# Kernel tuning notes

Measured on AMD Instinct MI355X. Metric: run time of the kernel, lower is better.

The kernel has to match this reference:

```python
import jax, jax.numpy as jnp
import numpy as np

B, S, H, L, V = 32, 128, 1024, 2, 32000


def setup_inputs() -> dict:
    key = jax.random.key(0)
    ks = jax.random.split(key, 9)
    scale = 1.0 / np.sqrt(H)
    return {
        "x": jax.random.randint(ks[0], (B, 1), 0, V),
        "hidden": jax.random.normal(ks[1], (L, B, H), jnp.float32) * 0.1,
        "cell": jax.random.normal(ks[2], (L, B, H), jnp.float32) * 0.1,
        "target": jax.random.randint(ks[3], (B, S), 0, V),
        "tf_ratio": 1,  # teacher forcing always on -> deterministic
        "emb": jax.random.normal(ks[4], (V, H), jnp.float32) * 0.02,
        "w_ih": jax.random.normal(ks[5], (L, 4 * H, H), jnp.float32) * scale,
        "w_hh": jax.random.normal(ks[6], (L, 4 * H, H), jnp.float32) * scale,
        "b_ih": jax.random.normal(ks[7], (L, 4 * H), jnp.float32) * scale,
        "b_hh": jax.random.normal(ks[8], (L, 4 * H), jnp.float32) * scale,
    }


def _lstm_decode(tokens, h0, c0, emb, w_ih, w_hh, b_ih, b_hh):
    # tokens: [B,S] int; embed all teacher-forced inputs at once
    x_seq = emb[tokens]                      # [B,S,H]
    x_tbh = jnp.swapaxes(x_seq, 0, 1)        # [S,B,H]
    n_layers = h0.shape[0]

    def step(carry, x_t):
        h, c = carry                         # each [L,B,H]
        inp = x_t                            # [B,H]
        hs, cs = [], []
        for l in range(n_layers):
            # PyTorch gate order: i, f, g, o
            z = inp @ w_ih[l].T + h[l] @ w_hh[l].T + b_ih[l] + b_hh[l]
            i, f, g, o = jnp.split(z, 4, axis=-1)
            c_new = jax.nn.sigmoid(f) * c[l] + jax.nn.sigmoid(i) * jnp.tanh(g)
            h_new = jax.nn.sigmoid(o) * jnp.tanh(c_new)
            hs.append(h_new)
            cs.append(c_new)
            inp = h_new
        return (jnp.stack(hs), jnp.stack(cs)), inp

    _, outs = jax.lax.scan(step, (h0, c0), x_tbh)  # outs: [S,B,H]
    out = jnp.swapaxes(outs, 0, 1)                 # [B,S,H]
    # tied-weight projection to vocab
    return jnp.einsum("bsh,vh->bsv", out, emb)     # [B,S,V]


def reference(x, hidden, cell, target, tf_ratio, emb, w_ih, w_hh, b_ih, b_hh):
    # tf_ratio == 1: step 0 consumes x, step i>=1 consumes target[:, i]
    tokens = jnp.concatenate([x, target[:, 1:]], axis=1)  # [B,S]
    return _lstm_decode(tokens, hidden, cell, emb, w_ih, w_hh, b_ih, b_hh)
```

## Files before the change

### kernel.cpp

```cpp
#include <hip/hip_runtime.h>
#include <stdint.h>


typedef __attribute__((ext_vector_type(8))) short short8;
typedef __attribute__((ext_vector_type(4))) float f32x4;

#define MFMA16(a, b, c) __builtin_amdgcn_mfma_f32_16x16x32_bf16((a), (b), (c), 0, 0, 0)

__device__ __forceinline__ unsigned short f2bf(float f) {
  union { float f; unsigned int u; } v; v.f = f;
  unsigned int u = v.u;
  return (unsigned short)((u + 0x7fffu + ((u >> 16) & 1u)) >> 16);
}

__device__ __forceinline__ void gload_lds16(const unsigned short* g, unsigned short* l) {
  __builtin_amdgcn_global_load_lds(
      (const __attribute__((address_space(1))) void*)g,
      (__attribute__((address_space(3))) void*)l, 16, 0, 0);
}

__device__ __forceinline__ void st_u32_dev(unsigned* p, unsigned v) {
  __hip_atomic_store(p, v, __ATOMIC_RELAXED, __HIP_MEMORY_SCOPE_AGENT);
}
__device__ __forceinline__ unsigned ld_u32_dev(const unsigned* p) {
  return __hip_atomic_load(p, __ATOMIC_RELAXED, __HIP_MEMORY_SCOPE_AGENT);
}


__global__ void cvt_bf16_k(const float* __restrict__ s, unsigned short* __restrict__ d, int n4) {
  int i = blockIdx.x * blockDim.x + threadIdx.x;
  int st = gridDim.x * blockDim.x;
  for (; i < n4; i += st) {
    float4 v = ((const float4*)s)[i];
    ushort4 o;
    o.x = f2bf(v.x); o.y = f2bf(v.y); o.z = f2bf(v.z); o.w = f2bf(v.w);
    ((ushort4*)d)[i] = o;
  }
}

__global__ void bias_sum_k(const float* __restrict__ a, const float* __restrict__ b,
                           float* __restrict__ o, int n) {
  int i = blockIdx.x * blockDim.x + threadIdx.x;
  if (i < n) o[i] = a[i] + b[i];
}

__global__ void embed_k(const int* __restrict__ x, const int* __restrict__ tgt,
                        const float* __restrict__ emb, unsigned short* __restrict__ xseq) {
  int row = blockIdx.x;
  int t = row >> 5, b = row & 31;
  int tok = (t == 0) ? x[b] : tgt[b * 128 + t];
  const float4* e = (const float4*)(emb + (size_t)tok * 1024);
  ushort4* o = (ushort4*)(xseq + (size_t)row * 1024);
  int i = threadIdx.x;
  float4 v = e[i];
  ushort4 u;
  u.x = f2bf(v.x); u.y = f2bf(v.y); u.z = f2bf(v.z); u.w = f2bf(v.w);
  o[i] = u;
}


__global__ __launch_bounds__(256, 2) void gemm_bf16_k(
    const unsigned short* __restrict__ A, const unsigned short* __restrict__ B,
    float* __restrict__ C, const float* __restrict__ bias, int N) {
  __shared__ __align__(16) unsigned short smem[32768];
  const int tid = threadIdx.x;
  const int lane = tid & 63;
  const int w = tid >> 6;
  const int wm = w >> 1, wn = w & 1;
  const int xcd = blockIdx.x & 7;
  const int idx = blockIdx.x >> 3;
  const int nBase = (idx >> 2) * 128;
  const int mBase = (xcd * 4 + (idx & 3)) * 128;
  const int lr = lane & 15, lk = lane >> 4;
  const int K = 1024;

  const int srow = tid >> 3;
  const int scol = (tid & 7) ^ (srow & 7);
  const int wchunk = tid & 192;

  f32x4 acc[4][4];
#pragma unroll
  for (int i = 0; i < 4; ++i)
#pragma unroll
    for (int j = 0; j < 4; ++j) acc[i][j] = (f32x4){0.f, 0.f, 0.f, 0.f};

  const unsigned short* Ag = A + (size_t)mBase * K;
  const unsigned short* Bg = B + (size_t)nBase * K;

  auto stage = [&](int buf, int kt) {
    unsigned short* Ab = smem + buf * 16384;
    unsigned short* Bb = Ab + 8192;
#pragma unroll
    for (int r = 0; r < 4; ++r) {
      int row = r * 32 + srow;
      const unsigned short* ga = Ag + (size_t)row * K + kt * 64 + scol * 8;
      const unsigned short* gb = Bg + (size_t)row * K + kt * 64 + scol * 8;
      gload_lds16(ga, &Ab[(r * 256 + wchunk) * 8]);
      gload_lds16(gb, &Bb[(r * 256 + wchunk) * 8]);
    }
  };

  stage(0, 0);
  __syncthreads();
  for (int kt = 0; kt < 16; ++kt) {
    int cur = kt & 1;
    if (kt < 15) stage(cur ^ 1, kt + 1);
    const unsigned short* Ac = smem + cur * 16384;
    const unsigned short* Bc = Ac + 8192;
#pragma unroll
    for (int ks = 0; ks < 2; ++ks) {
      short8 a[4], b[4];
#pragma unroll
      for (int mf = 0; mf < 4; ++mf) {
        int row = wm * 64 + mf * 16 + lr;
        int cc = (ks * 4 + lk) ^ (row & 7);
        a[mf] = *(const short8*)&Ac[row * 64 + cc * 8];
      }
#pragma unroll
      for (int nf = 0; nf < 4; ++nf) {
        int row = wn * 64 + nf * 16 + lr;
        int cc = (ks * 4 + lk) ^ (row & 7);
        b[nf] = *(const short8*)&Bc[row * 64 + cc * 8];
      }
#pragma unroll
      for (int mf = 0; mf < 4; ++mf)
#pragma unroll
        for (int nf = 0; nf < 4; ++nf)
          acc[mf][nf] = MFMA16(a[mf], b[nf], acc[mf][nf]);
    }
    __syncthreads();
  }

  float* cst = (float*)smem;
#pragma unroll
  for (int r = 0; r < 4; ++r) {
    __syncthreads();
#pragma unroll
    for (int nf = 0; nf < 4; ++nf) {
      int col = wn * 64 + nf * 16 + lr;
      float bv = bias ? bias[nBase + col] : 0.f;
#pragma unroll
      for (int i = 0; i < 4; ++i)
        cst[(wm * 16 + lk * 4 + i) * 132 + col] = acc[r][nf][i] + bv;
    }
    __syncthreads();
#pragma unroll
    for (int pss = 0; pss < 4; ++pss) {
      int idxq = pss * 256 + tid;
      int rl = idxq >> 5, cq = idxq & 31;
      int grow = mBase + (rl >> 4) * 64 + r * 16 + (rl & 15);
      f32x4 v = *(const f32x4*)&cst[rl * 132 + cq * 4];
      __builtin_nontemporal_store(v, (f32x4*)&C[(size_t)grow * N + nBase + cq * 4]);
    }
  }
}


struct PParams {
  const float* zx0;
  const unsigned short* whh0;
  const unsigned short* wih1;
  const unsigned short* whh1;
  const float* bsum1;
  const float* cell;
  unsigned short* h0hist;
  const unsigned short* h1init;
  unsigned short* outb;
  unsigned int* slots0;
  unsigned int* slots1;
};

__global__ __launch_bounds__(512, 1) void lstm_persist_k(PParams P) {
  const int tid = threadIdx.x;
  const int lane = tid & 63;
  const int w = tid >> 6;
  const int lr = lane & 15, lkk = lane >> 4;

  __shared__ __align__(16) unsigned short wlds[65536];
  __shared__ float zraw[4608];

  if (blockIdx.x < 64) {
    const int u0 = blockIdx.x * 16;
    const int m = w >> 2;
    const int gp = (w >> 1) & 1;
    const int kh = w & 1;
    const int g0 = gp * 2, g1 = gp * 2 + 1;

    for (int f = w; f < 128; f += 8) {
      int gg = f >> 5, kc = f & 31;
      const unsigned short* src =
          P.whh0 + (size_t)(gg * 1024 + u0 + lr) * 1024 + kc * 32 + lkk * 8;
      *(short8*)&wlds[f * 512 + lane * 8] = *(const short8*)src;
    }
    const int fb = tid >> 3;
    const int jp = tid & 7;
    float creg[2] = {0.f, 0.f};
    if (tid < 256) {
      creg[0] = P.cell[fb * 1024 + u0 + 2 * jp];
      creg[1] = P.cell[fb * 1024 + u0 + 2 * jp + 1];
    }
    __syncthreads();

    for (int i = 0; i < 128; ++i) {
      if (i > 0 && tid < 64) {
        const unsigned tgt = (unsigned)i;
        while (true) {
          unsigned v = ld_u32_dev(&P.slots0[tid * 32]);
          if (__all(v >= tgt)) break;
          __builtin_amdgcn_s_sleep(1);
        }
      }
      __syncthreads();

      float2 zr[4];
      if (tid < 256) {
        const float2* br = (const float2*)(P.zx0 + (size_t)i * 131072 + fb * 4096 + u0 + 2 * jp);
#pragma unroll
        for (int q = 0; q < 4; ++q) zr[q] = br[q * 512];
      }
      f32x4 acc0 = {0.f, 0.f, 0.f, 0.f}, acc1 = {0.f, 0.f, 0.f, 0.f};
      const unsigned short* ap =
          P.h0hist + (size_t)i * 32768 + (size_t)(m * 16 + lr) * 1024 + kh * 512 + lkk * 8;
#pragma unroll
      for (int g4 = 0; g4 < 2; ++g4) {
        short8 a[8];
#pragma unroll
        for (int q = 0; q < 8; ++q) a[q] = *(const short8*)(ap + (g4 * 8 + q) * 32);
#pragma unroll
        for (int q = 0; q < 8; ++q) {
          int kc = kh * 16 + g4 * 8 + q;
          short8 b0 = *(const short8*)&wlds[(g0 * 32 + kc) * 512 + lane * 8];
          short8 b1 = *(const short8*)&wlds[(g1 * 32 + kc) * 512 + lane * 8];
          acc0 = MFMA16(a[q], b0, acc0);
          acc1 = MFMA16(a[q], b1, acc1);
        }
      }
#pragma unroll
      for (int j = 0; j < 4; ++j) {
        zraw[(kh * 32 + m * 16 + lkk * 4 + j) * 72 + g0 * 16 + lr] = acc0[j];
        zraw[(kh * 32 + m * 16 + lkk * 4 + j) * 72 + g1 * 16 + lr] = acc1[j];
      }
      __syncthreads();

      if (tid < 256) {
        unsigned hv = 0;
#pragma unroll
        for (int u = 0; u < 2; ++u) {
          int j = 2 * jp + u;
          float zi = zraw[fb * 72 + j]      + zraw[(32 + fb) * 72 + j]      + ((u == 0) ? zr[0].x : zr[0].y);
          float zf = zraw[fb * 72 + 16 + j] + zraw[(32 + fb) * 72 + 16 + j] + ((u == 0) ? zr[1].x : zr[1].y);
          float zg = zraw[fb * 72 + 32 + j] + zraw[(32 + fb) * 72 + 32 + j] + ((u == 0) ? zr[2].x : zr[2].y);
          float zo = zraw[fb * 72 + 48 + j] + zraw[(32 + fb) * 72 + 48 + j] + ((u == 0) ? zr[3].x : zr[3].y);
          float ii = 1.f / (1.f + __expf(-zi));
          float ff = 1.f / (1.f + __expf(-zf));
          float gg = tanhf(zg);
          float oo = 1.f / (1.f + __expf(-zo));
          float cn = ff * creg[u] + ii * gg;
          creg[u] = cn;
          float hn = oo * tanhf(cn);
          hv |= ((unsigned)f2bf(hn)) << (16 * u);
        }
        st_u32_dev((unsigned*)&P.h0hist[(size_t)(i + 1) * 32768 + fb * 1024 + u0 + 2 * jp], hv);
      }
      __syncthreads();
      if (tid == 0) st_u32_dev(&P.slots0[blockIdx.x * 32], (unsigned)(i + 1));
    }
  } else {
    const int u0 = (blockIdx.x - 64) * 8;
    const int slot = blockIdx.x - 64;
    const int mat = w >> 2;
    const int m = (w >> 1) & 1;
    const int kh = w & 1;

    for (int f = w; f < 128; f += 8) {
      int matf = f >> 6, nt = (f >> 5) & 1, kc = f & 31;
      int rr = nt * 16 + lr;
      int gate = rr >> 3, unit = rr & 7;
      const unsigned short* Wm = matf ? P.whh1 : P.wih1;
      const unsigned short* src =
          Wm + (size_t)(gate * 1024 + u0 + unit) * 1024 + kc * 32 + lkk * 8;
      *(short8*)&wlds[f * 512 + lane * 8] = *(const short8*)src;
    }
    const int fb = tid >> 2;
    const int jp = tid & 3;
    float creg[2] = {0.f, 0.f};
    float brg[4][2];
    if (tid < 128) {
      creg[0] = P.cell[32768 + fb * 1024 + u0 + 2 * jp];
      creg[1] = P.cell[32768 + fb * 1024 + u0 + 2 * jp + 1];
#pragma unroll
      for (int q = 0; q < 4; ++q) {
        brg[q][0] = P.bsum1[q * 1024 + u0 + 2 * jp];
        brg[q][1] = P.bsum1[q * 1024 + u0 + 2 * jp + 1];
      }
    }
    __syncthreads();

    for (int i = 1; i <= 128; ++i) {
      if (tid < 64) {
        const unsigned t0 = (unsigned)i, t1 = (unsigned)(i - 1);
        while (true) {
          bool ok = ld_u32_dev(&P.slots0[tid * 32]) >= t0;
          if (i > 1) {
            ok = ok && ld_u32_dev(&P.slots1[tid * 32]) >= t1
                    && ld_u32_dev(&P.slots1[(tid + 64) * 32]) >= t1;
          }
          if (__all(ok)) break;
          __builtin_amdgcn_s_sleep(2);
        }
      }
      __syncthreads();

      f32x4 acc0 = {0.f, 0.f, 0.f, 0.f}, acc1 = {0.f, 0.f, 0.f, 0.f};
      const unsigned short* ap;
      if (mat == 0) {
        ap = P.h0hist + (size_t)i * 32768 + (size_t)(m * 16 + lr) * 1024 + kh * 512 + lkk * 8;
      } else {
        size_t h1s = (i == 1) ? 1024 : 131072;
        const unsigned short* h1b =
            (i == 1) ? P.h1init : (P.outb + (size_t)(i - 2) * 1024);
        ap = h1b + (size_t)(m * 16 + lr) * h1s + kh * 512 + lkk * 8;
      }
#pragma unroll
      for (int g4 = 0; g4 < 2; ++g4) {
        short8 a[8];
#pragma unroll
        for (int q = 0; q < 8; ++q) a[q] = *(const short8*)(ap + (g4 * 8 + q) * 32);
#pragma unroll
        for (int q = 0; q < 8; ++q) {
          int kc = kh * 16 + g4 * 8 + q;
          short8 b0 = *(const short8*)&wlds[(mat * 64 + 0 * 32 + kc) * 512 + lane * 8];
          short8 b1 = *(const short8*)&wlds[(mat * 64 + 1 * 32 + kc) * 512 + lane * 8];
          acc0 = MFMA16(a[q], b0, acc0);
          acc1 = MFMA16(a[q], b1, acc1);
        }
      }
      float* zp = zraw + (mat * 2 + kh) * 1152;
#pragma unroll
      for (int j = 0; j < 4; ++j) {
        zp[(m * 16 + lkk * 4 + j) * 36 + lr] = acc0[j];
        zp[(m * 16 + lkk * 4 + j) * 36 + 16 + lr] = acc1[j];
      }
      __syncthreads();

      if (tid < 128) {
        unsigned hv = 0;
#pragma unroll
        for (int u = 0; u < 2; ++u) {
          int j = 2 * jp + u;
          float z4[4];
#pragma unroll
          for (int q = 0; q < 4; ++q) {
            z4[q] = zraw[fb * 36 + q * 8 + j] + zraw[1152 + fb * 36 + q * 8 + j]
                  + zraw[2304 + fb * 36 + q * 8 + j] + zraw[3456 + fb * 36 + q * 8 + j]
                  + brg[q][u];
          }
          float ii = 1.f / (1.f + __expf(-z4[0]));
          float ff = 1.f / (1.f + __expf(-z4[1]));
          float gg = tanhf(z4[2]);
          float oo = 1.f / (1.f + __expf(-z4[3]));
          float cn = ff * creg[u] + ii * gg;
          creg[u] = cn;
          float hn = oo * tanhf(cn);
          hv |= ((unsigned)f2bf(hn)) << (16 * u);
        }
        st_u32_dev((unsigned*)&P.outb[(size_t)fb * 131072 + (size_t)(i - 1) * 1024 + u0 + 2 * jp], hv);
      }
      __syncthreads();
      if (tid == 0) st_u32_dev(&P.slots1[slot * 32], (unsigned)i);
    }
  }
}


extern "C" void kernel_launch(void* const* d_in, const int* in_sizes, int n_in,
                              void* d_out, int out_size, void* d_ws, size_t ws_size,
                              hipStream_t stream) {
  const int*   x      = (const int*)d_in[0];
  const float* hidden = (const float*)d_in[1];
  const float* cell   = (const float*)d_in[2];
  const int*   target = (const int*)d_in[3];
  const float* emb    = (const float*)d_in[5];
  const float* w_ih   = (const float*)d_in[6];
  const float* w_hh   = (const float*)d_in[7];
  const float* b_ih   = (const float*)d_in[8];
  const float* b_hh   = (const float*)d_in[9];
  float* out = (float*)d_out;
  char* ws = (char*)d_ws;

  unsigned short* emb_bf  = (unsigned short*)(ws);
  unsigned short* wih0_bf = (unsigned short*)(ws + 65536000);
  unsigned short* whh_bf  = (unsigned short*)(ws + 73924608);
  unsigned short* wih1_bf = (unsigned short*)(ws + 90701824);
  float*          bsum    = (float*)(ws + 99090432);
  unsigned short* outb    = (unsigned short*)(ws + 99123200);
  unsigned int*   barmem  = (unsigned int*)(ws + 107511808);
  float*          zx0    = (float*)((char*)d_out);
  unsigned short* xseq   = (unsigned short*)((char*)d_out + 67108864);
  unsigned short* h0hist = (unsigned short*)((char*)d_out + 75497472);
  unsigned short* h1init = (unsigned short*)((char*)d_out + 83951616);

  hipMemsetAsync(barmem, 0, 32768, stream);
  cvt_bf16_k<<<2048, 256, 0, stream>>>(emb, emb_bf, 8192000);
  cvt_bf16_k<<<1024, 256, 0, stream>>>(w_ih, wih0_bf, 1048576);
  cvt_bf16_k<<<2048, 256, 0, stream>>>(w_hh, whh_bf, 2097152);
  cvt_bf16_k<<<1024, 256, 0, stream>>>(w_ih + 4194304, wih1_bf, 1048576);
  cvt_bf16_k<<<32, 256, 0, stream>>>(hidden, h0hist, 8192);
  cvt_bf16_k<<<32, 256, 0, stream>>>(hidden + 32768, h1init, 8192);
  bias_sum_k<<<32, 256, 0, stream>>>(b_ih, b_hh, bsum, 8192);
  embed_k<<<4096, 256, 0, stream>>>(x, target, emb, xseq);

  gemm_bf16_k<<<1024, 256, 0, stream>>>(xseq, wih0_bf, zx0, bsum, 4096);

  PParams pp;
  pp.zx0 = zx0;
  pp.whh0 = whh_bf;
  pp.wih1 = wih1_bf;
  pp.whh1 = whh_bf + 4194304;
  pp.bsum1 = bsum + 4096;
  pp.cell = cell;
  pp.h0hist = h0hist;
  pp.h1init = h1init;
  pp.outb = outb;
  pp.slots0 = barmem;
  pp.slots1 = barmem + 2048;
  lstm_persist_k<<<192, 512, 0, stream>>>(pp);

  gemm_bf16_k<<<8000, 256, 0, stream>>>(outb, emb_bf, out, nullptr, 32000);
}
```

Before: 1.191 ms.

## Fuse vocab projection into persistent LSTM kernel via work queue overlap

```diff
diff --git a/kernel.cpp b/kernel.cpp
--- a/kernel.cpp
+++ b/kernel.cpp
@@ -61,7 +61,7 @@
 
 __global__ __launch_bounds__(256, 2) void gemm_bf16_k(
     const unsigned short* __restrict__ A, const unsigned short* __restrict__ B,
-    float* __restrict__ C, const float* __restrict__ bias, int N) {
+    float* __restrict__ C, const float* __restrict__ bias, int N, int permC) {
   __shared__ __align__(16) unsigned short smem[32768];
   const int tid = threadIdx.x;
   const int lane = tid & 63;
@@ -93,10 +93,8 @@
 #pragma unroll
     for (int r = 0; r < 4; ++r) {
       int row = r * 32 + srow;
-      const unsigned short* ga = Ag + (size_t)row * K + kt * 64 + scol * 8;
-      const unsigned short* gb = Bg + (size_t)row * K + kt * 64 + scol * 8;
-      gload_lds16(ga, &Ab[(r * 256 + wchunk) * 8]);
-      gload_lds16(gb, &Bb[(r * 256 + wchunk) * 8]);
+      gload_lds16(Ag + (size_t)row * K + kt * 64 + scol * 8, &Ab[(r * 256 + wchunk) * 8]);
+      gload_lds16(Bg + (size_t)row * K + kt * 64 + scol * 8, &Bb[(r * 256 + wchunk) * 8]);
     }
   };
 
@@ -148,9 +146,10 @@
     for (int pss = 0; pss < 4; ++pss) {
       int idxq = pss * 256 + tid;
       int rl = idxq >> 5, cq = idxq & 31;
-      int grow = mBase + (rl >> 4) * 64 + r * 16 + (rl & 15);
+      int ar = mBase + (rl >> 4) * 64 + r * 16 + (rl & 15);
+      int cr = permC ? ((ar & 31) * 128 + (ar >> 5)) : ar;
       f32x4 v = *(const f32x4*)&cst[rl * 132 + cq * 4];
-      __builtin_nontemporal_store(v, (f32x4*)&C[(size_t)grow * N + nBase + cq * 4]);
+      __builtin_nontemporal_store(v, (f32x4*)&C[(size_t)cr * N + nBase + cq * 4]);
     }
   }
 }
@@ -168,7 +167,107 @@
   unsigned short* outb;
   unsigned int* slots0;
   unsigned int* slots1;
+  unsigned int* queue;
+  const unsigned short* embB;
+  float* outC;
+  int njobs;
 };
+
+__device__ __forceinline__ void proj_tile(int j, bool valid, int ltid, char* smbase,
+                                          const unsigned short* Aout,
+                                          const unsigned short* Bemb, float* C) {
+  const int mB = j / 250, nB = j % 250;
+  const int mBase = mB * 128, nBase = nB * 128;
+  const int lane = ltid & 63;
+  const int w4 = ltid >> 6;
+  const int wm = w4 >> 1, wn = w4 & 1;
+  const int lr = lane & 15, lk = lane >> 4;
+  const int srow = ltid >> 3;
+  const int scol = (ltid & 7) ^ (srow & 7);
+  const int wchunk = ltid & 192;
+  unsigned short* smem = (unsigned short*)smbase;
+
+  f32x4 acc[4][4];
+#pragma unroll
+  for (int i = 0; i < 4; ++i)
+#pragma unroll
+    for (int q = 0; q < 4; ++q) acc[i][q] = (f32x4){0.f, 0.f, 0.f, 0.f};
+
+  const unsigned short* Ag = Aout + (size_t)mBase * 1024;
+  const unsigned short* Bg = Bemb + (size_t)nBase * 1024;
+
+  auto stage = [&](int buf, int kt) {
+    if (!valid) return;
+    unsigned short* Ab = smem + buf * 16384;
+    unsigned short* Bb = Ab + 8192;
+#pragma unroll
+    for (int r = 0; r < 4; ++r) {
+      int row = r * 32 + srow;
+      gload_lds16(Ag + (size_t)row * 1024 + kt * 64 + scol * 8, &Ab[(r * 256 + wchunk) * 8]);
+      gload_lds16(Bg + (size_t)row * 1024 + kt * 64 + scol * 8, &Bb[(r * 256 + wchunk) * 8]);
+    }
+  };
+
+  stage(0, 0);
+  __syncthreads();
+  for (int kt = 0; kt < 16; ++kt) {
+    int cur = kt & 1;
+    if (kt < 15) stage(cur ^ 1, kt + 1);
+    const unsigned short* Ac = smem + cur * 16384;
+    const unsigned short* Bc = Ac + 8192;
+    if (valid) {
+#pragma unroll
+      for (int ks = 0; ks < 2; ++ks) {
+        short8 a[4], b[4];
+#pragma unroll
+        for (int mf = 0; mf < 4; ++mf) {
+          int row = wm * 64 + mf * 16 + lr;
+          int cc = (ks * 4 + lk) ^ (row & 7);
+          a[mf] = *(const short8*)&Ac[row * 64 + cc * 8];
+        }
+#pragma unroll
+        for (int nf = 0; nf < 4; ++nf) {
+          int row = wn * 64 + nf * 16 + lr;
+          int cc = (ks * 4 + lk) ^ (row & 7);
+          b[nf] = *(const short8*)&Bc[row * 64 + cc * 8];
+        }
+#pragma unroll
+        for (int mf = 0; mf < 4; ++mf)
+#pragma unroll
+          for (int nf = 0; nf < 4; ++nf)
+            acc[mf][nf] = MFMA16(a[mf], b[nf], acc[mf][nf]);
+      }
+    }
+    __syncthreads();
+  }
+
+  float* cst = (float*)smem;
+#pragma unroll
+  for (int r = 0; r < 4; ++r) {
+    __syncthreads();
+    if (valid) {
+#pragma unroll
+      for (int nf = 0; nf < 4; ++nf) {
+        int col = wn * 64 + nf * 16 + lr;
+#pragma unroll
+        for (int i = 0; i < 4; ++i)
+          cst[(wm * 16 + lk * 4 + i) * 132 + col] = acc[r][nf][i];
+      }
+    }
+    __syncthreads();
+    if (valid) {
+#pragma unroll
+      for (int pss = 0; pss < 4; ++pss) {
+        int idxq = pss * 256 + ltid;
+        int rl = idxq >> 5, cq = idxq & 31;
+        int ar = mBase + (rl >> 4) * 64 + r * 16 + (rl & 15);
+        int cr = (ar & 31) * 128 + (ar >> 5);
+        f32x4 v = *(const f32x4*)&cst[rl * 132 + cq * 4];
+        __builtin_nontemporal_store(v, (f32x4*)&C[(size_t)cr * 32000 + nBase + cq * 4]);
+      }
+    }
+  }
+}
 
 __global__ __launch_bounds__(512, 1) void lstm_persist_k(PParams P) {
   const int tid = threadIdx.x;
@@ -176,8 +275,10 @@
   const int w = tid >> 6;
   const int lr = lane & 15, lkk = lane >> 4;
 
-  __shared__ __align__(16) unsigned short wlds[65536];
-  __shared__ float zraw[4608];
+  __shared__ __align__(16) char pool[149504];
+  __shared__ int jbase;
+  unsigned short* wlds = (unsigned short*)pool;
+  float* zraw = (float*)(pool + 131072);
 
   if (blockIdx.x < 64) {
     const int u0 = blockIdx.x * 16;
@@ -265,7 +366,7 @@
       __syncthreads();
       if (tid == 0) st_u32_dev(&P.slots0[blockIdx.x * 32], (unsigned)(i + 1));
     }
-  } else {
+  } else if (blockIdx.x < 192) {
     const int u0 = (blockIdx.x - 64) * 8;
     const int slot = blockIdx.x - 64;
     const int mat = w >> 2;
@@ -316,10 +417,9 @@
       if (mat == 0) {
         ap = P.h0hist + (size_t)i * 32768 + (size_t)(m * 16 + lr) * 1024 + kh * 512 + lkk * 8;
       } else {
-        size_t h1s = (i == 1) ? 1024 : 131072;
         const unsigned short* h1b =
-            (i == 1) ? P.h1init : (P.outb + (size_t)(i - 2) * 1024);
-        ap = h1b + (size_t)(m * 16 + lr) * h1s + kh * 512 + lkk * 8;
+            (i == 1) ? P.h1init : (P.outb + (size_t)(i - 2) * 32768);
+        ap = h1b + (size_t)(m * 16 + lr) * 1024 + kh * 512 + lkk * 8;
       }
 #pragma unroll
       for (int g4 = 0; g4 < 2; ++g4) {
@@ -364,11 +464,37 @@
           float hn = oo * tanhf(cn);
           hv |= ((unsigned)f2bf(hn)) << (16 * u);
         }
-        st_u32_dev((unsigned*)&P.outb[(size_t)fb * 131072 + (size_t)(i - 1) * 1024 + u0 + 2 * jp], hv);
+        st_u32_dev((unsigned*)&P.outb[(size_t)(i - 1) * 32768 + fb * 1024 + u0 + 2 * jp], hv);
       }
       __syncthreads();
       if (tid == 0) st_u32_dev(&P.slots1[slot * 32], (unsigned)i);
     }
+  }
+
+  while (true) {
+    __syncthreads();
+    if (tid == 0)
+      jbase = (int)__hip_atomic_fetch_add(P.queue, 2u, __ATOMIC_RELAXED,
+                                          __HIP_MEMORY_SCOPE_AGENT);
+    __syncthreads();
+    int base = jbase;
+    if (base >= P.njobs) break;
+    int j = base + (tid >> 8);
+    bool valid = (j < P.njobs);
+    int jmax = (base + 1 < P.njobs) ? base + 1 : base;
+    int gateMB = jmax / 250;
+    if (tid < 64) {
+      unsigned tgt = (unsigned)(4 * gateMB + 4);
+      if (tgt > 128u) tgt = 128u;
+      while (true) {
+        bool ok = ld_u32_dev(&P.slots1[tid * 32]) >= tgt &&
+                  ld_u32_dev(&P.slots1[(tid + 64) * 32]) >= tgt;
+        if (__all(ok)) break;
+        __builtin_amdgcn_s_sleep(2);
+      }
+    }
+    __syncthreads();
+    proj_tile(j, valid, tid & 255, pool + (tid >> 8) * 65536, P.outb, P.embB, P.outC);
   }
 }
 
@@ -395,10 +521,16 @@
   float*          bsum    = (float*)(ws + 99090432);
   unsigned short* outb    = (unsigned short*)(ws + 99123200);
   unsigned int*   barmem  = (unsigned int*)(ws + 107511808);
-  float*          zx0    = (float*)((char*)d_out);
-  unsigned short* xseq   = (unsigned short*)((char*)d_out + 67108864);
-  unsigned short* h0hist = (unsigned short*)((char*)d_out + 75497472);
-  unsigned short* h1init = (unsigned short*)((char*)d_out + 83951616);
+  unsigned short* h1init  = (unsigned short*)(ws + 107544576);
+
+  const size_t WS_NEED = 107610112ull + 67108864ull + 8454144ull;
+  const bool rich = (ws_size >= WS_NEED);
+  float*          zx0    = rich ? (float*)(ws + 107610112)
+                                : (float*)d_out;
+  unsigned short* xseq   = rich ? (unsigned short*)d_out
+                                : (unsigned short*)((char*)d_out + 67108864);
+  unsigned short* h0hist = rich ? (unsigned short*)(ws + 174718976)
+                                : (unsigned short*)((char*)d_out + 75497472);
 
   hipMemsetAsync(barmem, 0, 32768, stream);
   cvt_bf16_k<<<2048, 256, 0, stream>>>(emb, emb_bf, 8192000);
@@ -410,7 +542,7 @@
   bias_sum_k<<<32, 256, 0, stream>>>(b_ih, b_hh, bsum, 8192);
   embed_k<<<4096, 256, 0, stream>>>(x, target, emb, xseq);
 
-  gemm_bf16_k<<<1024, 256, 0, stream>>>(xseq, wih0_bf, zx0, bsum, 4096);
+  gemm_bf16_k<<<1024, 256, 0, stream>>>(xseq, wih0_bf, zx0, bsum, 4096, 0);
 
   PParams pp;
   pp.zx0 = zx0;
@@ -424,7 +556,13 @@
   pp.outb = outb;
   pp.slots0 = barmem;
   pp.slots1 = barmem + 2048;
-  lstm_persist_k<<<192, 512, 0, stream>>>(pp);
-
-  gemm_bf16_k<<<8000, 256, 0, stream>>>(outb, emb_bf, out, nullptr, 32000);
-}
+  pp.queue = barmem + 6144;
+  pp.embB = emb_bf;
+  pp.outC = out;
+  pp.njobs = rich ? 8000 : 0;
+  lstm_persist_k<<<rich ? 256 : 192, 512, 0, stream>>>(pp);
+
+  if (!rich) {
+    gemm_bf16_k<<<8000, 256, 0, stream>>>(outb, emb_bf, out, nullptr, 32000, 1);
+  }
+}
```

New measurement: 1.084 ms. -9.0%, faster.
